# Performance work log

Measured on AMD Instinct MI355X. Metric: run time of the kernel, lower is better.

## Reference

```python
import jax, jax.numpy as jnp
import numpy as np

B, C, T, K = 64, 12, 2048, 2048
LMAX = 11            # max kernel length among {7,9,11}
CMAX = C - 1         # torch.randint(1, C) -> at most C-1 selected channels
PL = 1024            # left pad: covers max 'same' left pad = (dil*(len-1))//2 <= (T-1)//2
PR = 3412            # right pad: covers zero-weight padded taps (LMAX-1)*dil_max
A = 7.0              # softppv_param


def setup_inputs() -> dict:
    rng = np.random.default_rng(0)
    klens = rng.choice(np.array([7, 9, 11]), size=K)
    nch = rng.integers(1, C, size=K)  # 1..C-1 channels per kernel
    weights = np.zeros((K, CMAX, LMAX), np.float32)
    ch_idx = np.zeros((K, CMAX), np.int32)
    dils = np.zeros(K, np.int32)
    offs = np.zeros(K, np.int32)
    olens = np.zeros(K, np.int32)
    for k in range(K):
        n, L = int(nch[k]), int(klens[k])
        ch_idx[k, :n] = rng.permutation(C)[:n]
        w = rng.standard_normal((n, L)).astype(np.float32)
        w -= w.mean(axis=1, keepdims=True)  # per-channel mean-centering as in torch init
        weights[k, :n, :L] = w
        d = int(2.0 ** rng.uniform(0.0, np.log2((T - 1) / (L - 1))))
        dils[k] = d
        if rng.integers(0, 2) == 0:  # padding='same' (torch: left=total//2, right=rest)
            offs[k] = PL - (d * (L - 1)) // 2
            olens[k] = T
        else:                        # padding='valid'
            offs[k] = PL
            olens[k] = T - d * (L - 1)
    biases = rng.uniform(0.0, 1.0, size=K).astype(np.float32)
    x = jax.random.normal(jax.random.key(0), (B, C, T), jnp.float32)
    return {
        "x": x,
        "weights": jnp.asarray(weights),
        "biases": jnp.asarray(biases),
        "ch_idx": jnp.asarray(ch_idx),
        "dils": jnp.asarray(dils),
        "offs": jnp.asarray(offs),
        "olens": jnp.asarray(olens),
    }


def reference(x, weights, biases, ch_idx, dils, offs, olens):
    # x: (B, C, T). Zero-pad time axis once so every (same/valid, dilation) variant
    # becomes a pure gather with a per-kernel offset; zero-padded weight taps/channels
    # contribute nothing, so padded gathers are harmless.
    xpad = jnp.pad(x, ((0, 0), (0, 0), (PL, PR)))
    t = jnp.arange(T)
    l = jnp.arange(LMAX)

    def step(_, p):
        W, b, ch, d, off, olen = p
        pos = off + t[:, None] + l[None, :] * d            # (T, LMAX) tap positions
        Xg = xpad[:, ch, :][:, :, pos]                     # (B, CMAX, T, LMAX)
        y = jnp.einsum('bctl,cl->bt', Xg, W) + b           # cross-correlation + bias
        mask = t < olen                                    # valid output positions
        ppv = jnp.sum(jax.nn.sigmoid(A * y - 3.0) * mask, axis=-1) / olen
        mx = jnp.max(jnp.where(mask, y, -jnp.inf), axis=-1)
        return None, (ppv, mx)

    _, (ppvs, mxs) = jax.lax.scan(step, None, (weights, biases, ch_idx, dils, offs, olens))
    # torch concatenates [ppv_k, max_k] per kernel along the feature axis -> (B, 2K)
    return jnp.stack([ppvs.T, mxs.T], axis=-1).reshape(x.shape[0], 2 * K)
```

## Files before the change

kernel.cpp:

```cpp
#include <hip/hip_runtime.h>
#include <math.h>

#define B_SZ   64
#define C_SZ   12
#define T_SZ   2048
#define K_SZ   2048
#define LMAX   11
#define CMAX   11
#define NPAIR  6
#define PL_PAD 1024
#define A_PARAM 7.0f

#define NW     8
#define BLOCK_MAIN (NW * 64)
#define R      8

typedef _Float16 h2 __attribute__((ext_vector_type(2)));

__device__ __forceinline__ float fdot2f(unsigned w, unsigned v, float acc) {
    return __builtin_amdgcn_fdot2(__builtin_bit_cast(h2, w),
                                  __builtin_bit_cast(h2, v), acc, false);
}

__global__ __launch_bounds__(256) void trh_kernel(const float* __restrict__ x,
                                                  unsigned short* __restrict__ xT) {
    const int c    = blockIdx.x;
    const int lane = threadIdx.x & 63;
    const int wid  = threadIdx.x >> 6;
    const int t0   = blockIdx.y * 128 + wid * 32;
    const float* xrow = x + ((size_t)lane * C_SZ + c) * T_SZ + t0;
    unsigned short* dst = xT + ((size_t)c * T_SZ + t0) * 64 + lane;
    #pragma unroll 8
    for (int i = 0; i < 32; ++i) {
        const _Float16 h = (_Float16)xrow[i];
        dst[i * 64] = __builtin_bit_cast(unsigned short, h);
    }
}

__global__ __launch_bounds__(1024) void sched_kernel(const float* __restrict__ w,
                                                     const int* __restrict__ olens,
                                                     unsigned* __restrict__ perm) {
    __shared__ unsigned key[K_SZ];
    const int tid = threadIdx.x;

    for (int k = tid; k < K_SZ; k += 1024) {
        const float* wk = w + (size_t)k * (CMAX * LMAX);
        int n = 0, L = 0;
        for (int e = 0; e < CMAX * LMAX; ++e) {
            if (wk[e] != 0.0f) {
                const int c = e / LMAX, l = e % LMAX;
                n = max(n, c + 1);
                L = max(L, l + 1);
            }
        }
        const unsigned cost = (unsigned)(n * L) * (unsigned)((olens[k] + 127) >> 7);
        key[k] = (cost << 11) | (unsigned)k;
    }
    __syncthreads();

    for (int ksz = 2; ksz <= K_SZ; ksz <<= 1) {
        for (int j = ksz >> 1; j > 0; j >>= 1) {
            for (int i = tid; i < K_SZ; i += 1024) {
                const int ixj = i ^ j;
                if (ixj > i) {
                    const unsigned a = key[i], b = key[ixj];
                    const bool sw = ((i & ksz) == 0) ? (a < b) : (a > b);
                    if (sw) { key[i] = b; key[ixj] = a; }
                }
            }
            __syncthreads();
        }
    }
    for (int i = tid; i < K_SZ; i += 1024)
        perm[i] = key[i] & 0x7FFu;
}

template<int LC>
__device__ __forceinline__ void conv_all(
    const unsigned short* __restrict__ xT,
    const int*      __restrict__ sCh,
    const unsigned  (* __restrict__ sWp)[LMAX],
    int npair, int d, int offr, int olen, float bias,
    int lane, int wid, float& psum, float& pmax)
{
    constexpr int NV = R + LC - 1;

    const int nj   = (olen + d - 1) / d;
    const int njb  = (nj + R - 1) / R;
    const int S    = (d >= 64) ? 1 : ((64 + d - 1) / d);
    const int len  = (njb + S - 1) / S;
    const int nunits = d * S;

    for (int u = wid; u < nunits; u += NW) {
        int q, seg;
        if (S == 1) { q = u; seg = 0; }
        else        { q = u % d; seg = u / d; }
        const int jb0 = seg * len;
        const int jb1 = min(njb, jb0 + len);

        for (int jb = jb0; jb < jb1; ++jb) {
            const int tq = q + jb * (R * d);
            if (tq >= olen) break;
            const int tpos0 = tq + offr;

            float y[R];
            #pragma unroll
            for (int r = 0; r < R; ++r) y[r] = bias;

            const bool fast = (tpos0 >= 0) && (tpos0 + (NV - 1) * d < T_SZ);

            if (fast) {
                for (int p = 0; p < npair; ++p) {
                    const int rbA = __builtin_amdgcn_readfirstlane(sCh[2*p  ] * T_SZ + tpos0);
                    const int rbB = __builtin_amdgcn_readfirstlane(sCh[2*p+1] * T_SZ + tpos0);
                    const unsigned short* rpA = xT + ((size_t)rbA << 6);
                    const unsigned short* rpB = xT + ((size_t)rbB << 6);

                    unsigned vp[NV];
                    #pragma unroll
                    for (int i = 0; i < NV; ++i) {
                        const unsigned a = rpA[lane];
                        const unsigned b = rpB[lane];
                        vp[i] = a | (b << 16);
                        rpA += (d << 6); rpB += (d << 6);
                    }

                    const unsigned* wrow = &sWp[p][0];
                    #pragma unroll
                    for (int l = 0; l < LC; ++l) {
                        const unsigned w = wrow[l];
                        #pragma unroll
                        for (int r = 0; r < R; ++r)
                            y[r] = fdot2f(w, vp[l + r], y[r]);
                    }
                }
            } else {
                for (int p = 0; p < npair; ++p) {
                    const int rbA = __builtin_amdgcn_readfirstlane(sCh[2*p  ] * T_SZ);
                    const int rbB = __builtin_amdgcn_readfirstlane(sCh[2*p+1] * T_SZ);
                    const unsigned short* rowA = xT + ((size_t)rbA << 6);
                    const unsigned short* rowB = xT + ((size_t)rbB << 6);

                    unsigned vp[NV];
                    #pragma unroll
                    for (int i = 0; i < NV; ++i) {
                        const int tp  = tpos0 + i * d;
                        const int tpc = min(max(tp, 0), T_SZ - 1);
                        const unsigned a = rowA[((size_t)tpc << 6) + lane];
                        const unsigned b = rowB[((size_t)tpc << 6) + lane];
                        const unsigned pk = a | (b << 16);
                        vp[i] = ((unsigned)tp < (unsigned)T_SZ) ? pk : 0u;
                    }

                    const unsigned* wrow = &sWp[p][0];
                    #pragma unroll
                    for (int l = 0; l < LC; ++l) {
                        const unsigned w = wrow[l];
                        #pragma unroll
                        for (int r = 0; r < R; ++r)
                            y[r] = fdot2f(w, vp[l + r], y[r]);
                    }
                }
            }

            #pragma unroll
            for (int r = 0; r < R; ++r) {
                const int t = tq + r * d;
                if (t < olen) {
                    psum += 1.0f / (1.0f + __expf(3.0f - A_PARAM * y[r]));
                    pmax  = fmaxf(pmax, y[r]);
                }
            }
        }
    }
}

__global__ __launch_bounds__(BLOCK_MAIN, 8) void rocket_tr(
    const unsigned short* __restrict__ xT,
    const unsigned* __restrict__ perm,
    const float* __restrict__ weights,
    const float* __restrict__ biases,
    const int*   __restrict__ ch_idx,
    const int*   __restrict__ dils,
    const int*   __restrict__ offs,
    const int*   __restrict__ olens,
    float*       __restrict__ out)
{
    __shared__ float    sW[CMAX][LMAX];
    __shared__ unsigned sWp[NPAIR][LMAX];
    __shared__ int      sCh[2 * NPAIR];
    __shared__ int      sMeta[2];
    __shared__ float    sP[NW][64];
    __shared__ float    sM[NW][64];

    const int k   = (int)perm[blockIdx.x];
    const int tid = threadIdx.x;

    if (tid < CMAX * LMAX)
        sW[tid / LMAX][tid % LMAX] = weights[(size_t)k * (CMAX * LMAX) + tid];
    if (tid < 2 * NPAIR)
        sCh[tid] = (tid < CMAX) ? ch_idx[(size_t)k * CMAX + tid] : 0;
    __syncthreads();

    if (tid < NPAIR * LMAX) {
        const int p = tid / LMAX;
        const int l = tid % LMAX;
        const float wA = sW[2 * p][l];
        const float wB = (2 * p + 1 < CMAX) ? sW[2 * p + 1][l] : 0.0f;
        h2 hh; hh.x = (_Float16)wA; hh.y = (_Float16)wB;
        sWp[p][l] = __builtin_bit_cast(unsigned, hh);
    }
    if (tid == 0) {
        int n = 0, L = 0;
        for (int c = 0; c < CMAX; ++c) {
            bool nz = false;
            for (int l = 0; l < LMAX; ++l) {
                if (sW[c][l] != 0.0f) { nz = true; if (l + 1 > L) L = l + 1; }
            }
            if (nz) n = c + 1;
        }
        sMeta[0] = n; sMeta[1] = L;
    }
    __syncthreads();

    const int   n     = sMeta[0];
    const int   L     = sMeta[1];
    const int   npair = (n + 1) >> 1;
    const int   d     = dils[k];
    const int   offr  = offs[k] - PL_PAD;
    const int   olen  = olens[k];
    const float bias  = biases[k];
    const int   lane  = tid & 63;
    const int   wid   = __builtin_amdgcn_readfirstlane(tid >> 6);

    float psum = 0.0f;
    float pmax = -INFINITY;

    if (L <= 7)
        conv_all<7 >(xT, sCh, sWp, npair, d, offr, olen, bias, lane, wid, psum, pmax);
    else if (L <= 9)
        conv_all<9 >(xT, sCh, sWp, npair, d, offr, olen, bias, lane, wid, psum, pmax);
    else
        conv_all<11>(xT, sCh, sWp, npair, d, offr, olen, bias, lane, wid, psum, pmax);

    sP[wid][lane] = psum;
    sM[wid][lane] = pmax;
    __syncthreads();

    if (tid < 64) {
        float s = 0.0f, m = -INFINITY;
        #pragma unroll
        for (int w = 0; w < NW; ++w) {
            s += sP[w][tid];
            m  = fmaxf(m, sM[w][tid]);
        }
        const float inv_olen = 1.0f / (float)olen;
        out[(size_t)tid * (2 * K_SZ) + 2 * k]     = s * inv_olen;
        out[(size_t)tid * (2 * K_SZ) + 2 * k + 1] = m;
    }
}

__global__ __launch_bounds__(256) void rocket_fallback(
    const float* __restrict__ x,
    const float* __restrict__ weights,
    const float* __restrict__ biases,
    const int*   __restrict__ ch_idx,
    const int*   __restrict__ dils,
    const int*   __restrict__ offs,
    const int*   __restrict__ olens,
    float*       __restrict__ out)
{
    __shared__ float sW[CMAX][LMAX];
    __shared__ int   sCh[CMAX];
    __shared__ float sRed[2][4];

    const int k   = blockIdx.x;
    const int tid = threadIdx.x;

    if (tid < CMAX * LMAX)
        sW[tid / LMAX][tid % LMAX] = weights[(size_t)k * (CMAX * LMAX) + tid];
    if (tid < CMAX)
        sCh[tid] = ch_idx[(size_t)k * CMAX + tid];
    __syncthreads();

    const int   d    = dils[k];
    const int   off  = offs[k] - PL_PAD;
    const int   olen = olens[k];
    const float bias = biases[k];
    const int   lane = tid & 63;
    const int   wid  = tid >> 6;

    for (int b = blockIdx.y; b < B_SZ; b += gridDim.y) {
        float psum = 0.0f, pmax = -INFINITY;
        for (int t = tid; t < T_SZ; t += 256) {
            float y = bias;
            for (int c = 0; c < CMAX; ++c) {
                const float* xb = x + ((size_t)b * C_SZ + sCh[c]) * T_SZ;
                int pos = off + t;
                for (int l = 0; l < LMAX; ++l) {
                    const float xv = ((unsigned)pos < (unsigned)T_SZ) ? xb[pos] : 0.0f;
                    y = fmaf(sW[c][l], xv, y);
                    pos += d;
                }
            }
            if (t < olen) {
                psum += 1.0f / (1.0f + __expf(3.0f - A_PARAM * y));
                pmax = fmaxf(pmax, y);
            }
        }
        for (int o = 32; o > 0; o >>= 1) {
            psum += __shfl_down(psum, o, 64);
            pmax  = fmaxf(pmax, __shfl_down(pmax, o, 64));
        }
        if (lane == 0) { sRed[0][wid] = psum; sRed[1][wid] = pmax; }
        __syncthreads();
        if (tid == 0) {
            const float s = sRed[0][0] + sRed[0][1] + sRed[0][2] + sRed[0][3];
            const float m = fmaxf(fmaxf(sRed[1][0], sRed[1][1]),
                                  fmaxf(sRed[1][2], sRed[1][3]));
            out[(size_t)b * (2 * K_SZ) + 2 * k]     = s / (float)olen;
            out[(size_t)b * (2 * K_SZ) + 2 * k + 1] = m;
        }
        __syncthreads();
    }
}

extern "C" void kernel_launch(void* const* d_in, const int* in_sizes, int n_in,
                              void* d_out, int out_size, void* d_ws, size_t ws_size,
                              hipStream_t stream) {
    const float* x       = (const float*)d_in[0];
    const float* weights = (const float*)d_in[1];
    const float* biases  = (const float*)d_in[2];
    const int*   ch_idx  = (const int*)  d_in[3];
    const int*   dils    = (const int*)  d_in[4];
    const int*   offs    = (const int*)  d_in[5];
    const int*   olens   = (const int*)  d_in[6];
    float*       out     = (float*)d_out;

    const size_t xt_bytes = (size_t)C_SZ * T_SZ * 64 * sizeof(unsigned short);
    const size_t need     = xt_bytes + K_SZ * sizeof(unsigned);

    if (ws_size >= need) {
        unsigned short* xT = (unsigned short*)d_ws;
        unsigned* perm     = (unsigned*)((char*)d_ws + xt_bytes);
        dim3 tgrid(C_SZ, T_SZ / 128);
        trh_kernel<<<tgrid, 256, 0, stream>>>(x, xT);
        sched_kernel<<<1, 1024, 0, stream>>>(weights, olens, perm);
        rocket_tr<<<K_SZ, BLOCK_MAIN, 0, stream>>>(xT, perm, weights, biases,
                                                   ch_idx, dils, offs, olens, out);
    } else {
        dim3 grid(K_SZ, 16);
        rocket_fallback<<<grid, 256, 0, stream>>>(x, weights, biases, ch_idx,
                                                  dils, offs, olens, out);
    }
}
```

Before: 749.1 us.

## Split each kernel's work across four blocks and combine partials in a second pass

Each convolution kernel's work units are now spread over four blocks instead of one. Each block writes partial sum/max values to workspace, and a new combine kernel reduces them and writes the normalized output. This is meant to fix load imbalance from long-tail kernels and raise parallelism. The launch bounds occupancy hint drops from 8 to 4, and half-word packing now uses v_perm. The cost is an extra launch, the partial-buffer traffic, and redundant per-block weight setup.

```diff
diff --git a/kernel.cpp b/kernel.cpp
--- a/kernel.cpp
+++ b/kernel.cpp
@@ -14,6 +14,7 @@
 #define NW     8
 #define BLOCK_MAIN (NW * 64)
 #define R      8
+#define SPL    4
 
 typedef _Float16 h2 __attribute__((ext_vector_type(2)));
 
@@ -80,7 +81,7 @@
     const unsigned short* __restrict__ xT,
     const int*      __restrict__ sCh,
     const unsigned  (* __restrict__ sWp)[LMAX],
-    int npair, int d, int offr, int olen, float bias,
+    int npair, int d, int offr, int olen, float bias, int sp,
     int lane, int wid, float& psum, float& pmax)
 {
     constexpr int NV = R + LC - 1;
@@ -91,7 +92,7 @@
     const int len  = (njb + S - 1) / S;
     const int nunits = d * S;
 
-    for (int u = wid; u < nunits; u += NW) {
+    for (int u = sp * NW + wid; u < nunits; u += NW * SPL) {
         int q, seg;
         if (S == 1) { q = u; seg = 0; }
         else        { q = u % d; seg = u / d; }
@@ -121,7 +122,7 @@
                     for (int i = 0; i < NV; ++i) {
                         const unsigned a = rpA[lane];
                         const unsigned b = rpB[lane];
-                        vp[i] = a | (b << 16);
+                        vp[i] = __builtin_amdgcn_perm(b, a, 0x05040100);
                         rpA += (d << 6); rpB += (d << 6);
                     }
 
@@ -148,7 +149,7 @@
                         const int tpc = min(max(tp, 0), T_SZ - 1);
                         const unsigned a = rowA[((size_t)tpc << 6) + lane];
                         const unsigned b = rowB[((size_t)tpc << 6) + lane];
-                        const unsigned pk = a | (b << 16);
+                        const unsigned pk = __builtin_amdgcn_perm(b, a, 0x05040100);
                         vp[i] = ((unsigned)tp < (unsigned)T_SZ) ? pk : 0u;
                     }
 
@@ -175,7 +176,7 @@
     }
 }
 
-__global__ __launch_bounds__(BLOCK_MAIN, 8) void rocket_tr(
+__global__ __launch_bounds__(BLOCK_MAIN, 4) void rocket_tr(
     const unsigned short* __restrict__ xT,
     const unsigned* __restrict__ perm,
     const float* __restrict__ weights,
@@ -184,7 +185,7 @@
     const int*   __restrict__ dils,
     const int*   __restrict__ offs,
     const int*   __restrict__ olens,
-    float*       __restrict__ out)
+    float*       __restrict__ part)
 {
     __shared__ float    sW[CMAX][LMAX];
     __shared__ unsigned sWp[NPAIR][LMAX];
@@ -193,8 +194,10 @@
     __shared__ float    sP[NW][64];
     __shared__ float    sM[NW][64];
 
-    const int k   = (int)perm[blockIdx.x];
-    const int tid = threadIdx.x;
+    const int kidx = blockIdx.x / SPL;
+    const int sp   = blockIdx.x % SPL;
+    const int k    = (int)perm[kidx];
+    const int tid  = threadIdx.x;
 
     if (tid < CMAX * LMAX)
         sW[tid / LMAX][tid % LMAX] = weights[(size_t)k * (CMAX * LMAX) + tid];
@@ -237,11 +240,11 @@
     float pmax = -INFINITY;
 
     if (L <= 7)
-        conv_all<7 >(xT, sCh, sWp, npair, d, offr, olen, bias, lane, wid, psum, pmax);
+        conv_all<7 >(xT, sCh, sWp, npair, d, offr, olen, bias, sp, lane, wid, psum, pmax);
     else if (L <= 9)
-        conv_all<9 >(xT, sCh, sWp, npair, d, offr, olen, bias, lane, wid, psum, pmax);
+        conv_all<9 >(xT, sCh, sWp, npair, d, offr, olen, bias, sp, lane, wid, psum, pmax);
     else
-        conv_all<11>(xT, sCh, sWp, npair, d, offr, olen, bias, lane, wid, psum, pmax);
+        conv_all<11>(xT, sCh, sWp, npair, d, offr, olen, bias, sp, lane, wid, psum, pmax);
 
     sP[wid][lane] = psum;
     sM[wid][lane] = pmax;
@@ -254,10 +257,30 @@
             s += sP[w][tid];
             m  = fmaxf(m, sM[w][tid]);
         }
-        const float inv_olen = 1.0f / (float)olen;
-        out[(size_t)tid * (2 * K_SZ) + 2 * k]     = s * inv_olen;
-        out[(size_t)tid * (2 * K_SZ) + 2 * k + 1] = m;
-    }
+        float* pp = part + ((size_t)k * SPL + sp) * 128;
+        pp[tid]      = s;
+        pp[64 + tid] = m;
+    }
+}
+
+__global__ __launch_bounds__(256) void combine_kernel(
+    const float* __restrict__ part,
+    const int*   __restrict__ olens,
+    float*       __restrict__ out)
+{
+    const int idx = blockIdx.x * 256 + threadIdx.x;
+    if (idx >= K_SZ * 64) return;
+    const int k = idx >> 6;
+    const int b = idx & 63;
+    const float* pp = part + (size_t)k * SPL * 128;
+    float s = 0.0f, m = -INFINITY;
+    #pragma unroll
+    for (int sp = 0; sp < SPL; ++sp) {
+        s += pp[sp * 128 + b];
+        m  = fmaxf(m, pp[sp * 128 + 64 + b]);
+    }
+    out[(size_t)b * (2 * K_SZ) + 2 * k]     = s / (float)olens[k];
+    out[(size_t)b * (2 * K_SZ) + 2 * k + 1] = m;
 }
 
 __global__ __launch_bounds__(256) void rocket_fallback(
@@ -337,17 +360,22 @@
     const int*   olens   = (const int*)  d_in[6];
     float*       out     = (float*)d_out;
 
-    const size_t xt_bytes = (size_t)C_SZ * T_SZ * 64 * sizeof(unsigned short);
-    const size_t need     = xt_bytes + K_SZ * sizeof(unsigned);
+    const size_t xt_bytes   = (size_t)C_SZ * T_SZ * 64 * sizeof(unsigned short);
+    const size_t perm_bytes = K_SZ * sizeof(unsigned);
+    const size_t part_bytes = (size_t)K_SZ * SPL * 128 * sizeof(float);
+    const size_t need       = xt_bytes + perm_bytes + part_bytes;
 
     if (ws_size >= need) {
         unsigned short* xT = (unsigned short*)d_ws;
         unsigned* perm     = (unsigned*)((char*)d_ws + xt_bytes);
+        float*    part     = (float*)((char*)d_ws + xt_bytes + perm_bytes);
         dim3 tgrid(C_SZ, T_SZ / 128);
         trh_kernel<<<tgrid, 256, 0, stream>>>(x, xT);
         sched_kernel<<<1, 1024, 0, stream>>>(weights, olens, perm);
-        rocket_tr<<<K_SZ, BLOCK_MAIN, 0, stream>>>(xT, perm, weights, biases,
-                                                   ch_idx, dils, offs, olens, out);
+        rocket_tr<<<K_SZ * SPL, BLOCK_MAIN, 0, stream>>>(xT, perm, weights,
+                                                         biases, ch_idx, dils,
+                                                         offs, olens, part);
+        combine_kernel<<<(K_SZ * 64 + 255) / 256, 256, 0, stream>>>(part, olens, out);
     } else {
         dim3 grid(K_SZ, 16);
         rocket_fallback<<<grid, 256, 0, stream>>>(x, weights, biases, ch_idx,
```

Result: faster. 678.0 us (-9.5%).
